# Kernel optimization log

Measured on AMD Instinct MI355X. Metric: run time of the kernel, lower is better.

Reference implementation:

```python
import math
import jax
import jax.numpy as jnp
import numpy as np
from jax import lax

B, L, D_MODEL, N_HEADS, C = 4, 2048, 512, 8, 1
D_HEAD = D_MODEL // N_HEADS


def setup_inputs() -> dict:
    key = jax.random.key(0)
    ks = jax.random.split(key, 7)
    s = 0.02  # stand-in for glorot init scale
    return {
        "queries": jax.random.normal(ks[0], (B, L, D_MODEL), jnp.float32),
        "keys": jax.random.normal(ks[1], (B, L, D_MODEL), jnp.float32),
        "values": jax.random.normal(ks[2], (B, L, D_MODEL), jnp.float32),
        "wq": jax.random.normal(ks[3], (D_MODEL, D_MODEL), jnp.float32) * s,
        "wk": jax.random.normal(ks[4], (D_MODEL, D_MODEL), jnp.float32) * s,
        "wv": jax.random.normal(ks[5], (D_MODEL, D_MODEL), jnp.float32) * s,
        "wo": jax.random.normal(ks[6], (D_MODEL, D_MODEL), jnp.float32) * s,
    }


def reference(queries, keys, values, wq, wk, wv, wo):
    b, len_q, _ = queries.shape
    len_k = keys.shape[1]
    # QKV projections, split into heads: [B, H, L, Dh]
    Q = (queries @ wq).reshape(b, len_q, N_HEADS, D_HEAD).transpose(0, 2, 1, 3)
    K = (keys @ wk).reshape(b, len_k, N_HEADS, D_HEAD).transpose(0, 2, 1, 3)
    V = (values @ wv).reshape(b, len_k, N_HEADS, D_HEAD).transpose(0, 2, 1, 3)
    # full O(L^2) correlation as in the original, then mean over heads & query idx
    corr = jnp.einsum("bhid,bhjd->bhij", Q, K)  # [B, H, Lq, Lk]
    mean_corr = corr.mean(axis=(1, 2))  # [B, Lk]
    # top-k delay selection (k = max(1, int(c * log(Lq))), static at trace time)
    k = max(1, int(C * math.log(max(2, len_q))))
    topk_vals, topk_idx = lax.top_k(mean_corr, k)  # [B, k]
    weights = jax.nn.softmax(topk_vals, axis=-1)  # [B, k]
    # vectorized circular roll: rolled[b,i,h,t,d] = V[b,h,(t+delay_bi) % L, d]
    idx = (jnp.arange(len_k)[None, None, :] + topk_idx[:, :, None]) % len_k  # [B,k,L]
    gathered = jnp.take_along_axis(
        V[:, None],  # [B, 1, H, L, Dh]
        idx[:, :, None, :, None],  # [B, k, 1, L, 1]
        axis=3,
    )  # [B, k, H, L, Dh]
    agg = jnp.einsum("bk,bkhld->bhld", weights.astype(V.dtype), gathered)
    out = agg.transpose(0, 2, 1, 3).reshape(b, len_q, D_MODEL) @ wo
    return out
```

## Files before the change

kernel.cpp:

```cpp
#include <hip/hip_runtime.h>
#include <hip/hip_bf16.h>

#define DMODEL 512
#define LEN 2048
#define NBATCH 4
#define TOPK 7
#define LDK 40

typedef __attribute__((ext_vector_type(8))) short short8;
typedef __attribute__((ext_vector_type(4))) float floatx4;

__device__ __forceinline__ float b2f(ushort h) {
  union { uint u; float f; } c; c.u = ((uint)h) << 16; return c.f;
}
__device__ __forceinline__ ushort f2b(float f) {
  union { float f; uint u; } c; c.f = f;
  uint u = c.u;
  uint r = (u + 0x7fffu + ((u >> 16) & 1u)) >> 16;
  return (ushort)r;
}

__device__ __forceinline__ float ld1(const void* p, size_t i, int bf) {
  return bf ? b2f(((const ushort*)p)[i]) : ((const float*)p)[i];
}
__device__ __forceinline__ void ld4v(const void* p, size_t i, int bf, float* o) {
  if (bf) {
    uint2 v = *(const uint2*)((const ushort*)p + i);
    const ushort* s = (const ushort*)&v;
#pragma unroll
    for (int j = 0; j < 4; ++j) o[j] = b2f(s[j]);
  } else {
    float4 a = *(const float4*)((const float*)p + i);
    o[0] = a.x; o[1] = a.y; o[2] = a.z; o[3] = a.w;
  }
}
__device__ __forceinline__ void ld8v(const void* p, size_t i, int bf, float* o) {
  if (bf) {
    uint4 v = *(const uint4*)((const ushort*)p + i);
    const ushort* s = (const ushort*)&v;
#pragma unroll
    for (int j = 0; j < 8; ++j) o[j] = b2f(s[j]);
  } else {
    float4 a = *(const float4*)((const float*)p + i);
    float4 b = *(const float4*)((const float*)p + i + 4);
    o[0] = a.x; o[1] = a.y; o[2] = a.z; o[3] = a.w;
    o[4] = b.x; o[5] = b.y; o[6] = b.z; o[7] = b.w;
  }
}

__device__ __forceinline__ int detect_bf16(const void* probe) {
  __shared__ int s_flag;
  int t = threadIdx.x;
  if (t < 64) {
    const uint4* p = (const uint4*)probe;
    uint4 a = p[t * 2];
    uint4 b = p[t * 2 + 1];
    uint w[8] = {a.x, a.y, a.z, a.w, b.x, b.y, b.z, b.w};
    int c = 0;
#pragma unroll
    for (int j = 0; j < 8; ++j) {
      uint e = (w[j] >> 7) & 0xFFu;
      c += (e < 90u || e > 140u) ? 1 : 0;
    }
#pragma unroll
    for (int off = 32; off > 0; off >>= 1) c += __shfl_down(c, off);
    if (t == 0) s_flag = (c < 50) ? 1 : 0;
  }
  __syncthreads();
  return s_flag;
}

__global__ __launch_bounds__(256) void prep_k(
    const void* __restrict__ queries, const void* __restrict__ values,
    const void* __restrict__ wq, const void* __restrict__ wk,
    const void* __restrict__ wv, const void* __restrict__ wo,
    float* __restrict__ P, ushort* __restrict__ VB,
    ushort* __restrict__ W2T, float* __restrict__ M) {
  __shared__ ushort As[64 * LDK];
  __shared__ ushort Bs[64 * LDK];
  __shared__ ushort Ts[64 * 72];
  int bf = detect_bf16(wq);
  int blk = blockIdx.x;
  int t = threadIdx.x;
  int w = t >> 6, lane = t & 63;
  int quad = lane >> 4, l16 = lane & 15;

  if (blk < 64) {
    int n0 = (blk & 7) * 64, m0 = (blk >> 3) * 64;
    floatx4 acc[4] = {{0,0,0,0},{0,0,0,0},{0,0,0,0},{0,0,0,0}};
    int am = t >> 2, ak = (t & 3) * 8;
    int kp = t >> 4, nb = (t & 15) * 4;
    for (int k0 = 0; k0 < DMODEL; k0 += 32) {
      float a8[8];
      ld8v(wv, (size_t)(m0 + am) * DMODEL + k0 + ak, bf, a8);
      union { ushort s[8]; uint4 v; } ap;
#pragma unroll
      for (int j = 0; j < 8; ++j) ap.s[j] = f2b(a8[j]);
      *(uint4*)(&As[am * LDK + ak]) = ap.v;
      float b0[4], b1[4];
      ld4v(wo, (size_t)(k0 + 2 * kp) * DMODEL + n0 + nb, bf, b0);
      ld4v(wo, (size_t)(k0 + 2 * kp + 1) * DMODEL + n0 + nb, bf, b1);
#pragma unroll
      for (int i = 0; i < 4; ++i) {
        ushort2 pr; pr.x = f2b(b0[i]); pr.y = f2b(b1[i]);
        *(ushort2*)(&Bs[(nb + i) * LDK + 2 * kp]) = pr;
      }
      __syncthreads();
      short8 af = *(const short8*)(&As[(w * 16 + l16) * LDK + quad * 8]);
#pragma unroll
      for (int c = 0; c < 4; ++c) {
        short8 bfr = *(const short8*)(&Bs[(c * 16 + l16) * LDK + quad * 8]);
        acc[c] = __builtin_amdgcn_mfma_f32_16x16x32_bf16(af, bfr, acc[c], 0, 0, 0);
      }
      __syncthreads();
    }
#pragma unroll
    for (int c = 0; c < 4; ++c) {
      int cl = c * 16 + l16;
#pragma unroll
      for (int r = 0; r < 4; ++r)
        Ts[cl * 72 + (w * 16 + quad * 4 + r)] = f2b(acc[c][r]);
    }
    __syncthreads();
    int nl = t >> 2, ch = t & 3;
    uint4 v0 = *(const uint4*)(&Ts[nl * 72 + ch * 16]);
    uint4 v1 = *(const uint4*)(&Ts[nl * 72 + ch * 16 + 8]);
    ushort* dst = W2T + (size_t)(n0 + nl) * DMODEL + m0 + ch * 16;
    *(uint4*)dst = v0;
    *(uint4*)(dst + 8) = v1;
  } else if (blk < 128) {
    int wb = blk - 64;
    int m0 = (wb >> 3) * 64, n0 = (wb & 7) * 64;
    floatx4 acc[4] = {{0,0,0,0},{0,0,0,0},{0,0,0,0},{0,0,0,0}};
    int am = t >> 2, ak = (t & 3) * 8;
    for (int k0 = 0; k0 < DMODEL; k0 += 32) {
      float a8[8], b8[8];
      ld8v(wk, (size_t)(m0 + am) * DMODEL + k0 + ak, bf, a8);
      ld8v(wq, (size_t)(n0 + am) * DMODEL + k0 + ak, bf, b8);
      union { ushort s[8]; uint4 v; } ap, bp;
#pragma unroll
      for (int j = 0; j < 8; ++j) { ap.s[j] = f2b(a8[j]); bp.s[j] = f2b(b8[j]); }
      *(uint4*)(&As[am * LDK + ak]) = ap.v;
      *(uint4*)(&Bs[am * LDK + ak]) = bp.v;
      __syncthreads();
      short8 af = *(const short8*)(&As[(w * 16 + l16) * LDK + quad * 8]);
#pragma unroll
      for (int c = 0; c < 4; ++c) {
        short8 bfr = *(const short8*)(&Bs[(c * 16 + l16) * LDK + quad * 8]);
        acc[c] = __builtin_amdgcn_mfma_f32_16x16x32_bf16(af, bfr, acc[c], 0, 0, 0);
      }
      __syncthreads();
    }
    int mrow = m0 + w * 16 + quad * 4;
#pragma unroll
    for (int c = 0; c < 4; ++c) {
      int col = n0 + c * 16 + l16;
#pragma unroll
      for (int r = 0; r < 4; ++r)
        M[(size_t)(mrow + r) * DMODEL + col] = acc[c][r];
    }
  } else if (blk < 384) {
    int idx = blk - 128;
    int b = idx >> 6, c = idx & 63;
    size_t base = (((size_t)b * LEN + (size_t)c * 32) << 9) + t;
    float a0 = 0.f, a1 = 0.f;
#pragma unroll 8
    for (int l = 0; l < 32; ++l) {
      a0 += ld1(queries, base + ((size_t)l << 9), bf);
      a1 += ld1(queries, base + ((size_t)l << 9) + 256, bf);
    }
    P[(size_t)idx * DMODEL + t] = a0;
    P[(size_t)idx * DMODEL + t + 256] = a1;
  } else {
    int r = (blk - 384) * 4 + w;
    float v[8];
    ld8v(values, ((size_t)r << 9) + lane * 8, bf, v);
    union { ushort o[8]; uint4 u; } pk;
#pragma unroll
    for (int j = 0; j < 8; ++j) pk.o[j] = f2b(v[j]);
    *(uint4*)(VB + ((size_t)r << 9) + lane * 8) = pk.u;
  }
}

__global__ __launch_bounds__(256) void u_all(
    const float* __restrict__ P, const float* __restrict__ M,
    float* __restrict__ U) {
  __shared__ float qs[DMODEL];
  int blk = blockIdx.x, t = threadIdx.x;
  int b = blk >> 5, g = blk & 31;
  int w = t >> 6, lane = t & 63;
  for (int d = t; d < DMODEL; d += 256) {
    float a = 0.f;
#pragma unroll
    for (int c = 0; c < 64; ++c) a += P[(size_t)(b * 64 + c) * DMODEL + d];
    qs[d] = a;
  }
  __syncthreads();
  const float* q8 = qs + lane * 8;
#pragma unroll
  for (int i = 0; i < 4; ++i) {
    int tt = g * 16 + w * 4 + i;
    const float* mr = M + (size_t)tt * DMODEL + lane * 8;
    float4 m0 = *(const float4*)mr;
    float4 m1 = *(const float4*)(mr + 4);
    float acc = m0.x * q8[0] + m0.y * q8[1] + m0.z * q8[2] + m0.w * q8[3]
              + m1.x * q8[4] + m1.y * q8[5] + m1.z * q8[6] + m1.w * q8[7];
#pragma unroll
    for (int off = 32; off > 0; off >>= 1) acc += __shfl_down(acc, off);
    if (lane == 0) U[(size_t)b * DMODEL + tt] = acc;
  }
}

__global__ __launch_bounds__(256) void mean_corr_k(
    const void* __restrict__ keys, const float* __restrict__ u,
    float* __restrict__ mc, const void* __restrict__ probe) {
  int bf = detect_bf16(probe);
  int wid = (blockIdx.x * 256 + threadIdx.x) >> 6;
  int lane = threadIdx.x & 63;
  int b = wid >> 11, j = wid & (LEN - 1);
  float kv[8];
  ld8v(keys, (((size_t)b * LEN + j) << 9) + lane * 8, bf, kv);
  const float* ub = u + (size_t)b * DMODEL + lane * 8;
  float acc = 0.f;
#pragma unroll
  for (int i = 0; i < 8; ++i) acc += kv[i] * ub[i];
#pragma unroll
  for (int off = 32; off > 0; off >>= 1) acc += __shfl_down(acc, off);
  if (lane == 0) mc[(size_t)b * LEN + j] = acc * (1.f / 16384.f);
}

__global__ __launch_bounds__(256) void topk_mix(
    const float* __restrict__ MC, const ushort* __restrict__ VB,
    ushort* __restrict__ Amix) {
  __shared__ float vals[LEN];
  __shared__ float rv[4];
  __shared__ int ri[4];
  __shared__ float bw[TOPK];
  __shared__ int biA[TOPK];
  __shared__ float wsm[8];
  __shared__ int dsm[8];
  int blk = blockIdx.x, t = threadIdx.x;
  int w = t >> 6, lane = t & 63;
  int b = blk >> 7;
  for (int i = t; i < LEN; i += 256) vals[i] = MC[(size_t)b * LEN + i];
  __syncthreads();
  for (int it = 0; it < TOPK; ++it) {
    float bv = -3.0e38f; int bi = 0;
#pragma unroll
    for (int c = 0; c < LEN / 256; ++c) {
      int i = t + c * 256;
      float v = vals[i];
      if (v > bv) { bv = v; bi = i; }
    }
#pragma unroll
    for (int off = 32; off > 0; off >>= 1) {
      float ov = __shfl_down(bv, off);
      int   oi = __shfl_down(bi, off);
      if (ov > bv || (ov == bv && oi < bi)) { bv = ov; bi = oi; }
    }
    if (lane == 0) { rv[w] = bv; ri[w] = bi; }
    __syncthreads();
    if (t == 0) {
      float fv = rv[0]; int fi = ri[0];
      for (int x = 1; x < 4; ++x)
        if (rv[x] > fv || (rv[x] == fv && ri[x] < fi)) { fv = rv[x]; fi = ri[x]; }
      bw[it] = fv; biA[it] = fi;
      vals[fi] = -3.0e38f;
    }
    __syncthreads();
  }
  if (t == 0) {
    float m = bw[0];
    float e[TOPK], s = 0.f;
#pragma unroll
    for (int i = 0; i < TOPK; ++i) { e[i] = __expf(bw[i] - m); s += e[i]; }
    float inv = 1.f / s;
#pragma unroll
    for (int i = 0; i < TOPK; ++i) { wsm[i] = e[i] * inv; dsm[i] = biA[i]; }
  }
  __syncthreads();
  float w7[TOPK]; int dl7[TOPK];
#pragma unroll
  for (int i = 0; i < TOPK; ++i) { w7[i] = wsm[i]; dl7[i] = dsm[i]; }
#pragma unroll
  for (int half = 0; half < 4; ++half) {
    int l = (blk & 127) * 16 + half * 4 + w;
    float acc[8] = {0,0,0,0,0,0,0,0};
#pragma unroll
    for (int i = 0; i < TOPK; ++i) {
      int src = (l + dl7[i]) & (LEN - 1);
      uint4 v = *(const uint4*)(VB + (((size_t)b * LEN + src) << 9) + lane * 8);
      const ushort* vs = (const ushort*)&v;
#pragma unroll
      for (int j = 0; j < 8; ++j) acc[j] += w7[i] * b2f(vs[j]);
    }
    union { ushort o[8]; uint4 v; } pk;
#pragma unroll
    for (int j = 0; j < 8; ++j) pk.o[j] = f2b(acc[j]);
    *(uint4*)(Amix + (((size_t)b * LEN + l) << 9) + lane * 8) = pk.v;
  }
}

__global__ __launch_bounds__(256) void gemm_out(
    const ushort* __restrict__ Amix, const ushort* __restrict__ W2T,
    void* __restrict__ out, const void* __restrict__ probe) {
  __shared__ ushort As[128 * LDK];
  __shared__ ushort Bs[128 * LDK];
  int bf = detect_bf16(probe);
  int t = threadIdx.x;
  int n0 = blockIdx.x * 128, m0 = blockIdx.y * 128;
  int w = t >> 6, lane = t & 63;
  int quad = lane >> 4, l16 = lane & 15;
  int wr = (w & 1) * 64, wc = (w >> 1) * 64;
  floatx4 acc[4][4];
#pragma unroll
  for (int r = 0; r < 4; ++r)
#pragma unroll
    for (int c = 0; c < 4; ++c) acc[r][c] = (floatx4){0, 0, 0, 0};
  int sr = t >> 2, sc = (t & 3) * 8;
  for (int k0 = 0; k0 < DMODEL; k0 += 32) {
    *(uint4*)(&As[sr * LDK + sc])        = *(const uint4*)(Amix + (size_t)(m0 + sr) * DMODEL + k0 + sc);
    *(uint4*)(&As[(sr + 64) * LDK + sc]) = *(const uint4*)(Amix + (size_t)(m0 + sr + 64) * DMODEL + k0 + sc);
    *(uint4*)(&Bs[sr * LDK + sc])        = *(const uint4*)(W2T + (size_t)(n0 + sr) * DMODEL + k0 + sc);
    *(uint4*)(&Bs[(sr + 64) * LDK + sc]) = *(const uint4*)(W2T + (size_t)(n0 + sr + 64) * DMODEL + k0 + sc);
    __syncthreads();
    short8 af[4], bfg[4];
#pragma unroll
    for (int r = 0; r < 4; ++r)
      af[r] = *(const short8*)(&As[(wr + r * 16 + l16) * LDK + quad * 8]);
#pragma unroll
    for (int c = 0; c < 4; ++c)
      bfg[c] = *(const short8*)(&Bs[(wc + c * 16 + l16) * LDK + quad * 8]);
#pragma unroll
    for (int r = 0; r < 4; ++r)
#pragma unroll
      for (int c = 0; c < 4; ++c)
        acc[r][c] = __builtin_amdgcn_mfma_f32_16x16x32_bf16(af[r], bfg[c], acc[r][c], 0, 0, 0);
    __syncthreads();
  }
#pragma unroll
  for (int r = 0; r < 4; ++r) {
    int row = m0 + wr + r * 16 + quad * 4;
#pragma unroll
    for (int c = 0; c < 4; ++c) {
      int col = n0 + wc + c * 16 + l16;
#pragma unroll
      for (int rr = 0; rr < 4; ++rr) {
        size_t oidx = (size_t)(row + rr) * DMODEL + col;
        float v = acc[r][c][rr];
        if (bf) ((ushort*)out)[oidx] = f2b(v);
        else    ((float*)out)[oidx] = v;
      }
    }
  }
}

extern "C" void kernel_launch(void* const* d_in, const int* in_sizes, int n_in,
                              void* d_out, int out_size, void* d_ws, size_t ws_size,
                              hipStream_t stream) {
  const void* queries = d_in[0];
  const void* keys    = d_in[1];
  const void* values  = d_in[2];
  const void* wq      = d_in[3];
  const void* wk      = d_in[4];
  const void* wv      = d_in[5];
  const void* wo      = d_in[6];

  char* ws = (char*)d_ws;
  float*  P    = (float*)(ws + 0);
  ushort* W2T  = (ushort*)(ws + 524288);
  float*  M    = (float*)(ws + 1048576);
  float*  U    = (float*)(ws + 2097152);
  float*  MC   = (float*)(ws + 2105344);
  ushort* VB   = (ushort*)(ws + 4194304);
  ushort* AMIX = (ushort*)(ws + 12582912);

  prep_k<<<2432, 256, 0, stream>>>(queries, values, wq, wk, wv, wo, P, VB, W2T, M);
  u_all<<<128, 256, 0, stream>>>(P, M, U);
  mean_corr_k<<<NBATCH * LEN / 4, 256, 0, stream>>>(keys, U, MC, wq);
  topk_mix<<<512, 256, 0, stream>>>(MC, VB, AMIX);
  gemm_out<<<dim3(4, 64), 256, 0, stream>>>(AMIX, W2T, d_out, wq);
}
```

Before: 155.2 us.

## Fuse top-k delay mixing into output GEMM A-tile loading

Merges the top-k selection and weighted circular-shift mixing into the output projection GEMM, so each GEMM block computes its own mixed A tile from V on the fly instead of reading a materialized Amix buffer. This removes one kernel launch and the write and read of the 8 MB intermediate. In exchange every GEMM block (256 of them, four per row tile) repeats the top-k search over 2048 values and the 7-way gather is redone once per N-tile, which quadruples the V gather traffic and adds serial top-k latency to each block.

```diff
diff --git a/kernel.cpp b/kernel.cpp
--- a/kernel.cpp
+++ b/kernel.cpp
@@ -229,88 +229,71 @@
   if (lane == 0) mc[(size_t)b * LEN + j] = acc * (1.f / 16384.f);
 }
 
-__global__ __launch_bounds__(256) void topk_mix(
+__global__ __launch_bounds__(256) void mixgemm2(
     const float* __restrict__ MC, const ushort* __restrict__ VB,
-    ushort* __restrict__ Amix) {
-  __shared__ float vals[LEN];
-  __shared__ float rv[4];
-  __shared__ int ri[4];
-  __shared__ float bw[TOPK];
-  __shared__ int biA[TOPK];
-  __shared__ float wsm[8];
-  __shared__ int dsm[8];
-  int blk = blockIdx.x, t = threadIdx.x;
-  int w = t >> 6, lane = t & 63;
-  int b = blk >> 7;
-  for (int i = t; i < LEN; i += 256) vals[i] = MC[(size_t)b * LEN + i];
-  __syncthreads();
-  for (int it = 0; it < TOPK; ++it) {
-    float bv = -3.0e38f; int bi = 0;
-#pragma unroll
-    for (int c = 0; c < LEN / 256; ++c) {
-      int i = t + c * 256;
-      float v = vals[i];
-      if (v > bv) { bv = v; bi = i; }
-    }
-#pragma unroll
-    for (int off = 32; off > 0; off >>= 1) {
-      float ov = __shfl_down(bv, off);
-      int   oi = __shfl_down(bi, off);
-      if (ov > bv || (ov == bv && oi < bi)) { bv = ov; bi = oi; }
-    }
-    if (lane == 0) { rv[w] = bv; ri[w] = bi; }
-    __syncthreads();
-    if (t == 0) {
-      float fv = rv[0]; int fi = ri[0];
-      for (int x = 1; x < 4; ++x)
-        if (rv[x] > fv || (rv[x] == fv && ri[x] < fi)) { fv = rv[x]; fi = ri[x]; }
-      bw[it] = fv; biA[it] = fi;
-      vals[fi] = -3.0e38f;
-    }
-    __syncthreads();
-  }
-  if (t == 0) {
-    float m = bw[0];
-    float e[TOPK], s = 0.f;
-#pragma unroll
-    for (int i = 0; i < TOPK; ++i) { e[i] = __expf(bw[i] - m); s += e[i]; }
-    float inv = 1.f / s;
-#pragma unroll
-    for (int i = 0; i < TOPK; ++i) { wsm[i] = e[i] * inv; dsm[i] = biA[i]; }
-  }
-  __syncthreads();
-  float w7[TOPK]; int dl7[TOPK];
-#pragma unroll
-  for (int i = 0; i < TOPK; ++i) { w7[i] = wsm[i]; dl7[i] = dsm[i]; }
-#pragma unroll
-  for (int half = 0; half < 4; ++half) {
-    int l = (blk & 127) * 16 + half * 4 + w;
-    float acc[8] = {0,0,0,0,0,0,0,0};
-#pragma unroll
-    for (int i = 0; i < TOPK; ++i) {
-      int src = (l + dl7[i]) & (LEN - 1);
-      uint4 v = *(const uint4*)(VB + (((size_t)b * LEN + src) << 9) + lane * 8);
-      const ushort* vs = (const ushort*)&v;
-#pragma unroll
-      for (int j = 0; j < 8; ++j) acc[j] += w7[i] * b2f(vs[j]);
-    }
-    union { ushort o[8]; uint4 v; } pk;
-#pragma unroll
-    for (int j = 0; j < 8; ++j) pk.o[j] = f2b(acc[j]);
-    *(uint4*)(Amix + (((size_t)b * LEN + l) << 9) + lane * 8) = pk.v;
-  }
-}
-
-__global__ __launch_bounds__(256) void gemm_out(
-    const ushort* __restrict__ Amix, const ushort* __restrict__ W2T,
-    void* __restrict__ out, const void* __restrict__ probe) {
-  __shared__ ushort As[128 * LDK];
-  __shared__ ushort Bs[128 * LDK];
+    const ushort* __restrict__ W2T, void* __restrict__ out,
+    const void* __restrict__ probe) {
+  __shared__ __align__(16) char smem[20480];
+  ushort* As = (ushort*)smem;
+  ushort* Bs = (ushort*)(smem + 10240);
   int bf = detect_bf16(probe);
   int t = threadIdx.x;
   int n0 = blockIdx.x * 128, m0 = blockIdx.y * 128;
+  int b = m0 >> 11;
   int w = t >> 6, lane = t & 63;
   int quad = lane >> 4, l16 = lane & 15;
+
+  float w7[TOPK]; int dl7[TOPK];
+  {
+    float* vals = (float*)smem;
+    float* rv  = (float*)(smem + 8192);
+    int*   ri  = (int*)  (smem + 8208);
+    float* bw  = (float*)(smem + 8224);
+    int*   biA = (int*)  (smem + 8256);
+    float* wsm = (float*)(smem + 8288);
+    int*   dsm = (int*)  (smem + 8320);
+    for (int i = t; i < LEN; i += 256) vals[i] = MC[(size_t)b * LEN + i];
+    __syncthreads();
+    for (int it = 0; it < TOPK; ++it) {
+      float bv = -3.0e38f; int bi = 0;
+#pragma unroll
+      for (int c = 0; c < LEN / 256; ++c) {
+        int i = t + c * 256;
+        float v = vals[i];
+        if (v > bv) { bv = v; bi = i; }
+      }
+#pragma unroll
+      for (int off = 32; off > 0; off >>= 1) {
+        float ov = __shfl_down(bv, off);
+        int   oi = __shfl_down(bi, off);
+        if (ov > bv || (ov == bv && oi < bi)) { bv = ov; bi = oi; }
+      }
+      if (lane == 0) { rv[w] = bv; ri[w] = bi; }
+      __syncthreads();
+      if (t == 0) {
+        float fv = rv[0]; int fi = ri[0];
+        for (int x = 1; x < 4; ++x)
+          if (rv[x] > fv || (rv[x] == fv && ri[x] < fi)) { fv = rv[x]; fi = ri[x]; }
+        bw[it] = fv; biA[it] = fi;
+        vals[fi] = -3.0e38f;
+      }
+      __syncthreads();
+    }
+    if (t == 0) {
+      float m = bw[0];
+      float e[TOPK], s = 0.f;
+#pragma unroll
+      for (int i = 0; i < TOPK; ++i) { e[i] = __expf(bw[i] - m); s += e[i]; }
+      float inv = 1.f / s;
+#pragma unroll
+      for (int i = 0; i < TOPK; ++i) { wsm[i] = e[i] * inv; dsm[i] = biA[i]; }
+    }
+    __syncthreads();
+#pragma unroll
+    for (int i = 0; i < TOPK; ++i) { w7[i] = wsm[i]; dl7[i] = dsm[i]; }
+    __syncthreads();
+  }
+
   int wr = (w & 1) * 64, wc = (w >> 1) * 64;
   floatx4 acc[4][4];
 #pragma unroll
@@ -318,9 +301,31 @@
 #pragma unroll
     for (int c = 0; c < 4; ++c) acc[r][c] = (floatx4){0, 0, 0, 0};
   int sr = t >> 2, sc = (t & 3) * 8;
+  int l_lo = (m0 & (LEN - 1)) + sr;
+  const ushort* VBb = VB + ((size_t)b * LEN << 9);
+
   for (int k0 = 0; k0 < DMODEL; k0 += 32) {
-    *(uint4*)(&As[sr * LDK + sc])        = *(const uint4*)(Amix + (size_t)(m0 + sr) * DMODEL + k0 + sc);
-    *(uint4*)(&As[(sr + 64) * LDK + sc]) = *(const uint4*)(Amix + (size_t)(m0 + sr + 64) * DMODEL + k0 + sc);
+    float a0[8] = {0,0,0,0,0,0,0,0}, a1[8] = {0,0,0,0,0,0,0,0};
+#pragma unroll
+    for (int i = 0; i < TOPK; ++i) {
+      int s0 = (l_lo + dl7[i]) & (LEN - 1);
+      int s1 = (l_lo + 64 + dl7[i]) & (LEN - 1);
+      uint4 v0 = *(const uint4*)(VBb + ((size_t)s0 << 9) + k0 + sc);
+      uint4 v1 = *(const uint4*)(VBb + ((size_t)s1 << 9) + k0 + sc);
+      const ushort* p0 = (const ushort*)&v0;
+      const ushort* p1 = (const ushort*)&v1;
+      float wi = w7[i];
+#pragma unroll
+      for (int j = 0; j < 8; ++j) {
+        a0[j] += wi * b2f(p0[j]);
+        a1[j] += wi * b2f(p1[j]);
+      }
+    }
+    union { ushort s[8]; uint4 v; } pk0, pk1;
+#pragma unroll
+    for (int j = 0; j < 8; ++j) { pk0.s[j] = f2b(a0[j]); pk1.s[j] = f2b(a1[j]); }
+    *(uint4*)(&As[sr * LDK + sc])        = pk0.v;
+    *(uint4*)(&As[(sr + 64) * LDK + sc]) = pk1.v;
     *(uint4*)(&Bs[sr * LDK + sc])        = *(const uint4*)(W2T + (size_t)(n0 + sr) * DMODEL + k0 + sc);
     *(uint4*)(&Bs[(sr + 64) * LDK + sc]) = *(const uint4*)(W2T + (size_t)(n0 + sr + 64) * DMODEL + k0 + sc);
     __syncthreads();
@@ -373,11 +378,9 @@
   float*  U    = (float*)(ws + 2097152);
   float*  MC   = (float*)(ws + 2105344);
   ushort* VB   = (ushort*)(ws + 4194304);
-  ushort* AMIX = (ushort*)(ws + 12582912);
 
   prep_k<<<2432, 256, 0, stream>>>(queries, values, wq, wk, wv, wo, P, VB, W2T, M);
   u_all<<<128, 256, 0, stream>>>(P, M, U);
   mean_corr_k<<<NBATCH * LEN / 4, 256, 0, stream>>>(keys, U, MC, wq);
-  topk_mix<<<512, 256, 0, stream>>>(MC, VB, AMIX);
-  gemm_out<<<dim3(4, 64), 256, 0, stream>>>(AMIX, W2T, d_out, wq);
-}
+  mixgemm2<<<dim3(4, 64), 256, 0, stream>>>(MC, VB, W2T, d_out, wq);
+}
```

Result: slower. 162.8 us (+4.9%).

## Project values before top-k mixing and fuse GEMM with u computation

Applied to the files above, without the earlier changes.

Because the weighted circular mix is linear, the output projection is applied to the bf16 values first (VB @ W2T) rather than to the mixed result. That GEMM runs in the same launch as the u-vector computation, one block type per branch, so it no longer waits on top-k selection. The top-k mix kernel then writes the final output directly in fp32 or bf16, removing the separate output GEMM launch and the Amix round trip. The GEMM also gains register prefetch of the next K tile, and its barriers are lighter (waiting only on LDS counters). The price is one extra rounding of the projected values to bf16 before mixing, which may change numerics slightly.

```diff
diff --git a/kernel.cpp b/kernel.cpp
--- a/kernel.cpp
+++ b/kernel.cpp
@@ -46,6 +46,11 @@
     o[0] = a.x; o[1] = a.y; o[2] = a.z; o[3] = a.w;
     o[4] = b.x; o[5] = b.y; o[6] = b.z; o[7] = b.w;
   }
+}
+
+__device__ __forceinline__ void block_sync_lds() {
+  asm volatile("s_waitcnt lgkmcnt(0)" ::: "memory");
+  __builtin_amdgcn_s_barrier();
 }
 
 __device__ __forceinline__ int detect_bf16(const void* probe) {
@@ -182,32 +187,92 @@
   }
 }
 
-__global__ __launch_bounds__(256) void u_all(
-    const float* __restrict__ P, const float* __restrict__ M,
-    float* __restrict__ U) {
-  __shared__ float qs[DMODEL];
+__global__ __launch_bounds__(256) void gemm_u(
+    const ushort* __restrict__ VB, const ushort* __restrict__ W2T,
+    ushort* __restrict__ VO, const float* __restrict__ P,
+    const float* __restrict__ M, float* __restrict__ U) {
+  __shared__ __align__(16) char smem[20480];
   int blk = blockIdx.x, t = threadIdx.x;
-  int b = blk >> 5, g = blk & 31;
   int w = t >> 6, lane = t & 63;
-  for (int d = t; d < DMODEL; d += 256) {
-    float a = 0.f;
-#pragma unroll
-    for (int c = 0; c < 64; ++c) a += P[(size_t)(b * 64 + c) * DMODEL + d];
-    qs[d] = a;
-  }
-  __syncthreads();
-  const float* q8 = qs + lane * 8;
-#pragma unroll
-  for (int i = 0; i < 4; ++i) {
-    int tt = g * 16 + w * 4 + i;
-    const float* mr = M + (size_t)tt * DMODEL + lane * 8;
-    float4 m0 = *(const float4*)mr;
-    float4 m1 = *(const float4*)(mr + 4);
-    float acc = m0.x * q8[0] + m0.y * q8[1] + m0.z * q8[2] + m0.w * q8[3]
-              + m1.x * q8[4] + m1.y * q8[5] + m1.z * q8[6] + m1.w * q8[7];
-#pragma unroll
-    for (int off = 32; off > 0; off >>= 1) acc += __shfl_down(acc, off);
-    if (lane == 0) U[(size_t)b * DMODEL + tt] = acc;
+
+  if (blk < 256) {
+    ushort* As = (ushort*)smem;
+    ushort* Bs = (ushort*)(smem + 10240);
+    int quad = lane >> 4, l16 = lane & 15;
+    int n0 = (blk >> 6) * 128, m0 = (blk & 63) * 128;
+    int wr = (w & 1) * 64, wc = (w >> 1) * 64;
+    floatx4 acc[4][4];
+#pragma unroll
+    for (int r = 0; r < 4; ++r)
+#pragma unroll
+      for (int c = 0; c < 4; ++c) acc[r][c] = (floatx4){0, 0, 0, 0};
+    int sr = t >> 2, sc = (t & 3) * 8;
+    const ushort* a0p = VB + (size_t)(m0 + sr) * DMODEL + sc;
+    const ushort* a1p = VB + (size_t)(m0 + sr + 64) * DMODEL + sc;
+    const ushort* b0p = W2T + (size_t)(n0 + sr) * DMODEL + sc;
+    const ushort* b1p = W2T + (size_t)(n0 + sr + 64) * DMODEL + sc;
+    uint4 ga0 = *(const uint4*)(a0p), ga1 = *(const uint4*)(a1p);
+    uint4 gb0 = *(const uint4*)(b0p), gb1 = *(const uint4*)(b1p);
+    for (int k0 = 0; k0 < DMODEL; k0 += 32) {
+      *(uint4*)(&As[sr * LDK + sc])        = ga0;
+      *(uint4*)(&As[(sr + 64) * LDK + sc]) = ga1;
+      *(uint4*)(&Bs[sr * LDK + sc])        = gb0;
+      *(uint4*)(&Bs[(sr + 64) * LDK + sc]) = gb1;
+      int kn = k0 + 32;
+      if (kn < DMODEL) {
+        ga0 = *(const uint4*)(a0p + kn); ga1 = *(const uint4*)(a1p + kn);
+        gb0 = *(const uint4*)(b0p + kn); gb1 = *(const uint4*)(b1p + kn);
+      }
+      block_sync_lds();
+      short8 af[4], bfg[4];
+#pragma unroll
+      for (int r = 0; r < 4; ++r)
+        af[r] = *(const short8*)(&As[(wr + r * 16 + l16) * LDK + quad * 8]);
+#pragma unroll
+      for (int c = 0; c < 4; ++c)
+        bfg[c] = *(const short8*)(&Bs[(wc + c * 16 + l16) * LDK + quad * 8]);
+#pragma unroll
+      for (int r = 0; r < 4; ++r)
+#pragma unroll
+        for (int c = 0; c < 4; ++c)
+          acc[r][c] = __builtin_amdgcn_mfma_f32_16x16x32_bf16(af[r], bfg[c], acc[r][c], 0, 0, 0);
+      block_sync_lds();
+    }
+#pragma unroll
+    for (int r = 0; r < 4; ++r) {
+      int row = m0 + wr + r * 16 + quad * 4;
+#pragma unroll
+      for (int c = 0; c < 4; ++c) {
+        int col = n0 + wc + c * 16 + l16;
+#pragma unroll
+        for (int rr = 0; rr < 4; ++rr)
+          VO[(size_t)(row + rr) * DMODEL + col] = f2b(acc[r][c][rr]);
+      }
+    }
+  } else {
+    float* qs = (float*)smem;
+    int ib = blk - 256;
+    int b = ib >> 5, g = ib & 31;
+    for (int d = t; d < DMODEL; d += 256) {
+      float a = 0.f;
+#pragma unroll
+      for (int c = 0; c < 64; ++c) a += P[(size_t)(b * 64 + c) * DMODEL + d];
+      qs[d] = a;
+    }
+    __syncthreads();
+    const float* q8 = qs + lane * 8;
+#pragma unroll
+    for (int i = 0; i < 4; ++i) {
+      int tt = g * 16 + w * 4 + i;
+      const float* mr = M + (size_t)tt * DMODEL + lane * 8;
+      float4 m0 = *(const float4*)mr;
+      float4 m1 = *(const float4*)(mr + 4);
+      float acc = m0.x * q8[0] + m0.y * q8[1] + m0.z * q8[2] + m0.w * q8[3]
+                + m1.x * q8[4] + m1.y * q8[5] + m1.z * q8[6] + m1.w * q8[7];
+#pragma unroll
+      for (int off = 32; off > 0; off >>= 1) acc += __shfl_down(acc, off);
+      if (lane == 0) U[(size_t)b * DMODEL + tt] = acc;
+    }
   }
 }
 
@@ -229,9 +294,9 @@
   if (lane == 0) mc[(size_t)b * LEN + j] = acc * (1.f / 16384.f);
 }
 
-__global__ __launch_bounds__(256) void topk_mix(
-    const float* __restrict__ MC, const ushort* __restrict__ VB,
-    ushort* __restrict__ Amix) {
+__global__ __launch_bounds__(256) void topk_mix_out(
+    const float* __restrict__ MC, const ushort* __restrict__ VO,
+    void* __restrict__ out, const void* __restrict__ probe) {
   __shared__ float vals[LEN];
   __shared__ float rv[4];
   __shared__ int ri[4];
@@ -239,9 +304,10 @@
   __shared__ int biA[TOPK];
   __shared__ float wsm[8];
   __shared__ int dsm[8];
+  int bf = detect_bf16(probe);
   int blk = blockIdx.x, t = threadIdx.x;
   int w = t >> 6, lane = t & 63;
-  int b = blk >> 7;
+  int b = blk & 3, g = blk >> 2;
   for (int i = t; i < LEN; i += 256) vals[i] = MC[(size_t)b * LEN + i];
   __syncthreads();
   for (int it = 0; it < TOPK; ++it) {
@@ -282,75 +348,30 @@
   float w7[TOPK]; int dl7[TOPK];
 #pragma unroll
   for (int i = 0; i < TOPK; ++i) { w7[i] = wsm[i]; dl7[i] = dsm[i]; }
-#pragma unroll
-  for (int half = 0; half < 4; ++half) {
-    int l = (blk & 127) * 16 + half * 4 + w;
+  const ushort* VOb = VO + ((size_t)b * LEN << 9);
+#pragma unroll
+  for (int p = 0; p < 4; ++p) {
+    int l = g * 16 + p * 4 + w;
     float acc[8] = {0,0,0,0,0,0,0,0};
 #pragma unroll
     for (int i = 0; i < TOPK; ++i) {
       int src = (l + dl7[i]) & (LEN - 1);
-      uint4 v = *(const uint4*)(VB + (((size_t)b * LEN + src) << 9) + lane * 8);
+      uint4 v = *(const uint4*)(VOb + ((size_t)src << 9) + lane * 8);
       const ushort* vs = (const ushort*)&v;
 #pragma unroll
       for (int j = 0; j < 8; ++j) acc[j] += w7[i] * b2f(vs[j]);
     }
-    union { ushort o[8]; uint4 v; } pk;
-#pragma unroll
-    for (int j = 0; j < 8; ++j) pk.o[j] = f2b(acc[j]);
-    *(uint4*)(Amix + (((size_t)b * LEN + l) << 9) + lane * 8) = pk.v;
-  }
-}
-
-__global__ __launch_bounds__(256) void gemm_out(
-    const ushort* __restrict__ Amix, const ushort* __restrict__ W2T,
-    void* __restrict__ out, const void* __restrict__ probe) {
-  __shared__ ushort As[128 * LDK];
-  __shared__ ushort Bs[128 * LDK];
-  int bf = detect_bf16(probe);
-  int t = threadIdx.x;
-  int n0 = blockIdx.x * 128, m0 = blockIdx.y * 128;
-  int w = t >> 6, lane = t & 63;
-  int quad = lane >> 4, l16 = lane & 15;
-  int wr = (w & 1) * 64, wc = (w >> 1) * 64;
-  floatx4 acc[4][4];
-#pragma unroll
-  for (int r = 0; r < 4; ++r)
-#pragma unroll
-    for (int c = 0; c < 4; ++c) acc[r][c] = (floatx4){0, 0, 0, 0};
-  int sr = t >> 2, sc = (t & 3) * 8;
-  for (int k0 = 0; k0 < DMODEL; k0 += 32) {
-    *(uint4*)(&As[sr * LDK + sc])        = *(const uint4*)(Amix + (size_t)(m0 + sr) * DMODEL + k0 + sc);
-    *(uint4*)(&As[(sr + 64) * LDK + sc]) = *(const uint4*)(Amix + (size_t)(m0 + sr + 64) * DMODEL + k0 + sc);
-    *(uint4*)(&Bs[sr * LDK + sc])        = *(const uint4*)(W2T + (size_t)(n0 + sr) * DMODEL + k0 + sc);
-    *(uint4*)(&Bs[(sr + 64) * LDK + sc]) = *(const uint4*)(W2T + (size_t)(n0 + sr + 64) * DMODEL + k0 + sc);
-    __syncthreads();
-    short8 af[4], bfg[4];
-#pragma unroll
-    for (int r = 0; r < 4; ++r)
-      af[r] = *(const short8*)(&As[(wr + r * 16 + l16) * LDK + quad * 8]);
-#pragma unroll
-    for (int c = 0; c < 4; ++c)
-      bfg[c] = *(const short8*)(&Bs[(wc + c * 16 + l16) * LDK + quad * 8]);
-#pragma unroll
-    for (int r = 0; r < 4; ++r)
-#pragma unroll
-      for (int c = 0; c < 4; ++c)
-        acc[r][c] = __builtin_amdgcn_mfma_f32_16x16x32_bf16(af[r], bfg[c], acc[r][c], 0, 0, 0);
-    __syncthreads();
-  }
-#pragma unroll
-  for (int r = 0; r < 4; ++r) {
-    int row = m0 + wr + r * 16 + quad * 4;
-#pragma unroll
-    for (int c = 0; c < 4; ++c) {
-      int col = n0 + wc + c * 16 + l16;
-#pragma unroll
-      for (int rr = 0; rr < 4; ++rr) {
-        size_t oidx = (size_t)(row + rr) * DMODEL + col;
-        float v = acc[r][c][rr];
-        if (bf) ((ushort*)out)[oidx] = f2b(v);
-        else    ((float*)out)[oidx] = v;
-      }
+    size_t oidx = (((size_t)b * LEN + l) << 9) + lane * 8;
+    if (bf) {
+      union { ushort o[8]; uint4 v; } pk;
+#pragma unroll
+      for (int j = 0; j < 8; ++j) pk.o[j] = f2b(acc[j]);
+      *(uint4*)((ushort*)out + oidx) = pk.v;
+    } else {
+      float4 f0 = {acc[0], acc[1], acc[2], acc[3]};
+      float4 f1 = {acc[4], acc[5], acc[6], acc[7]};
+      *(float4*)((float*)out + oidx) = f0;
+      *(float4*)((float*)out + oidx + 4) = f1;
     }
   }
 }
@@ -373,11 +394,10 @@
   float*  U    = (float*)(ws + 2097152);
   float*  MC   = (float*)(ws + 2105344);
   ushort* VB   = (ushort*)(ws + 4194304);
-  ushort* AMIX = (ushort*)(ws + 12582912);
+  ushort* VO   = (ushort*)(ws + 12582912);
 
   prep_k<<<2432, 256, 0, stream>>>(queries, values, wq, wk, wv, wo, P, VB, W2T, M);
-  u_all<<<128, 256, 0, stream>>>(P, M, U);
+  gemm_u<<<384, 256, 0, stream>>>(VB, W2T, VO, P, M, U);
   mean_corr_k<<<NBATCH * LEN / 4, 256, 0, stream>>>(keys, U, MC, wq);
-  topk_mix<<<512, 256, 0, stream>>>(MC, VB, AMIX);
-  gemm_out<<<dim3(4, 64), 256, 0, stream>>>(AMIX, W2T, d_out, wq);
-}
+  topk_mix_out<<<512, 256, 0, stream>>>(MC, VO, d_out, wq);
+}
```

Result: faster. 143.1 us, median of 2 (-7.8%).
